# Kernel tuning notes

Measured on AMD Instinct MI355X. Metric: run time of the kernel, lower is better.

The kernel has to match this reference:

```python
import jax, jax.numpy as jnp
import numpy as np
from jax.scipy.special import logsumexp

TEMPERATURE = 0.1
NEG_INF = -1e30


def _l2_normalize(x, eps=1e-12):
    # matches torch F.normalize(dim=1)
    n = jnp.sqrt(jnp.sum(x * x, axis=1, keepdims=True))
    return x / jnp.maximum(n, eps)


def _half_loss(out0, out1, diag):
    # sim matrices [N, N]
    sim_00 = jnp.einsum('nc,mc->nm', out0, out0) / TEMPERATURE
    sim_01 = jnp.einsum('nc,mc->nm', out0, out1) / TEMPERATURE
    positive_loss = -jnp.diagonal(sim_01)            # [N]
    # off-diagonal logsumexp per row (mask diag with -inf)
    neg_00 = logsumexp(jnp.where(diag, NEG_INF, sim_00), axis=1)
    neg_01 = logsumexp(jnp.where(diag, NEG_INF, sim_01), axis=1)
    return positive_loss.mean() + (neg_01 + neg_00).mean()


def setup_inputs() -> dict:
    key = jax.random.key(0)
    k0, k1 = jax.random.split(key)
    N, C = 8192, 128
    return {
        'img_rep': jax.random.normal(k0, (N, C), dtype=jnp.float32),
        'mol_rep': jax.random.normal(k1, (N, C), dtype=jnp.float32),
    }


def reference(img_rep, mol_rep):
    img = _l2_normalize(img_rep)
    mol = _l2_normalize(mol_rep)
    n = img.shape[0]
    diag = jnp.eye(n, dtype=bool)
    loss0 = _half_loss(img, mol, diag)  # mol_from_img
    loss1 = _half_loss(mol, img, diag)  # img_from_mol
    return 0.5 * (loss0 + loss1)
```

## Files before the change

kernel.cpp:

```cpp
#include <hip/hip_runtime.h>
#include <hip/hip_bf16.h>

typedef __attribute__((ext_vector_type(8))) short short8;
typedef __attribute__((ext_vector_type(4))) float floatx4;

#define N_ROWS 8192
#define C_DIM  128
#define CH     8
#define CHUNK  (N_ROWS / CH)
#define NIT    (CHUNK / 64)
#define KSCALE 14.426950408889634f
#define LN2    0.6931471805599453f

__device__ __forceinline__ unsigned int pack_bf16x2(float x, float y) {
    union { float f; unsigned int u; } a, b;
    a.f = x; b.f = y;
    unsigned int ra = a.u + 0x7FFFu + ((a.u >> 16) & 1u);
    unsigned int rb = b.u + 0x7FFFu + ((b.u >> 16) & 1u);
    return (ra >> 16) | ((rb >> 16) << 16);
}
__device__ __forceinline__ float bf2f(unsigned short s) {
    union { unsigned int u; float f; } x; x.u = ((unsigned int)s) << 16;
    return x.f;
}

__global__ __launch_bounds__(256) void norm_kernel(
    const float* __restrict__ img, const float* __restrict__ mol,
    unsigned short* __restrict__ W)
{
    int wave = threadIdx.x >> 6, lane = threadIdx.x & 63;
    int row = blockIdx.x * 4 + wave;
    const float* src = (row < N_ROWS) ? (img + (size_t)row * C_DIM)
                                      : (mol + (size_t)(row - N_ROWS) * C_DIM);
    float2 v = *reinterpret_cast<const float2*>(src + lane * 2);
    float ss = v.x * v.x + v.y * v.y;
    #pragma unroll
    for (int m = 1; m < 64; m <<= 1) ss += __shfl_xor(ss, m);
    float inv = rsqrtf(ss);
    ((unsigned int*)(W + (size_t)row * C_DIM))[lane] =
        pack_bf16x2(v.x * inv, v.y * inv);
}

__global__ __launch_bounds__(256) void pass_kernel(
    const unsigned short* __restrict__ W, float* __restrict__ SE)
{
    __shared__ unsigned short buf[2][64][128];
    int pass = blockIdx.z;
    const unsigned short* X = (pass < 2) ? W : W + (size_t)N_ROWS * C_DIM;
    const unsigned short* Y = (pass == 1 || pass == 2)
                                ? W + (size_t)N_ROWS * C_DIM : W;
    int lane = threadIdx.x & 63, wave = threadIdx.x >> 6;
    int l15 = lane & 15, lg = lane >> 4;
    int rbase = blockIdx.x * 128 + wave * 32;
    int cstart = blockIdx.y * CHUNK;

    short8 af[2][4];
    #pragma unroll
    for (int m = 0; m < 2; ++m)
        #pragma unroll
        for (int k = 0; k < 4; ++k)
            af[m][k] = *reinterpret_cast<const short8*>(
                X + (size_t)(rbase + m * 16 + l15) * C_DIM + k * 32 + lg * 8);

    auto stage = [&](int bsel, int jb) {
        #pragma unroll
        for (int i = 0; i < 4; ++i) {
            int c = i * 4 + wave;
            int r = c * 4 + lg;
            int s = l15 ^ (r & 7);
            const void* gsrc = (const char*)Y + (size_t)(jb + r) * 256 + s * 16;
            void* ldst = (char*)&buf[bsel][0][0] + c * 1024;
            __builtin_amdgcn_global_load_lds(
                (const __attribute__((address_space(1))) unsigned int*)gsrc,
                (__attribute__((address_space(3))) unsigned int*)ldst,
                16, 0, 0);
        }
    };

    float se[2][4] = {{0.f,0.f,0.f,0.f},{0.f,0.f,0.f,0.f}};

    stage(0, cstart);
    int cur = 0;
    for (int it = 0; it < NIT; ++it) {
        if (it + 1 < NIT) {
            stage(cur ^ 1, cstart + (it + 1) * 64);
            asm volatile("s_waitcnt vmcnt(4)" ::: "memory");
        } else {
            asm volatile("s_waitcnt vmcnt(0)" ::: "memory");
        }
        __builtin_amdgcn_s_barrier();
        asm volatile("" ::: "memory");

        #pragma unroll
        for (int n = 0; n < 4; ++n) {
            short8 bk[4];
            #pragma unroll
            for (int k = 0; k < 4; ++k) {
                int row = n * 16 + l15;
                int s = (k * 4 + lg) ^ (l15 & 7);
                bk[k] = *reinterpret_cast<const short8*>(
                    (const char*)&buf[cur][0][0] + row * 256 + s * 16);
            }
            #pragma unroll
            for (int m = 0; m < 2; ++m) {
                floatx4 acc = {0.f, 0.f, 0.f, 0.f};
                #pragma unroll
                for (int k = 0; k < 4; ++k)
                    acc = __builtin_amdgcn_mfma_f32_16x16x32_bf16(
                              af[m][k], bk[k], acc, 0, 0, 0);
                #pragma unroll
                for (int r = 0; r < 4; ++r)
                    se[m][r] += __builtin_amdgcn_exp2f(acc[r] * KSCALE - KSCALE);
            }
        }
        asm volatile("s_waitcnt lgkmcnt(0)" ::: "memory");
        __builtin_amdgcn_sched_barrier(0);
        __builtin_amdgcn_s_barrier();
        cur ^= 1;
    }

    float* SEp = SE + (size_t)pass * N_ROWS;
    #pragma unroll
    for (int m = 0; m < 2; ++m)
        #pragma unroll
        for (int r = 0; r < 4; ++r) {
            float s = se[m][r];
            s += __shfl_xor(s, 1);
            s += __shfl_xor(s, 2);
            s += __shfl_xor(s, 4);
            s += __shfl_xor(s, 8);
            if (l15 == 0)
                atomicAdd(&SEp[rbase + m * 16 + lg * 4 + r], s);
        }
}

__global__ __launch_bounds__(256) void finalize_kernel(
    const unsigned short* __restrict__ W, const float* __restrict__ SE,
    float* __restrict__ out)
{
    __shared__ float partial[4];
    int lane = threadIdx.x & 63, wave = threadIdx.x >> 6;
    int row = blockIdx.x * 4 + wave;
    const unsigned short* a = W + (size_t)row * C_DIM;
    const unsigned short* b = W + (size_t)(N_ROWS + row) * C_DIM;
    float a0 = bf2f(a[lane * 2]), a1 = bf2f(a[lane * 2 + 1]);
    float b0 = bf2f(b[lane * 2]), b1 = bf2f(b[lane * 2 + 1]);
    float d00 = a0 * a0 + a1 * a1;
    float d01 = a0 * b0 + a1 * b1;
    float d11 = b0 * b0 + b1 * b1;
    #pragma unroll
    for (int m = 1; m < 64; m <<= 1) {
        d00 += __shfl_xor(d00, m);
        d01 += __shfl_xor(d01, m);
        d11 += __shfl_xor(d11, m);
    }
    if (lane == 0) {
        float s0 = SE[0 * N_ROWS + row] - __builtin_amdgcn_exp2f(KSCALE * (d00 - 1.f));
        float s1 = SE[1 * N_ROWS + row] - __builtin_amdgcn_exp2f(KSCALE * (d01 - 1.f));
        float s2 = SE[2 * N_ROWS + row] - __builtin_amdgcn_exp2f(KSCALE * (d11 - 1.f));
        float s3 = SE[3 * N_ROWS + row] - __builtin_amdgcn_exp2f(KSCALE * (d01 - 1.f));
        float l0 = LN2 * __builtin_amdgcn_logf(s0) + 10.f;
        float l1 = LN2 * __builtin_amdgcn_logf(s1) + 10.f;
        float l2 = LN2 * __builtin_amdgcn_logf(s2) + 10.f;
        float l3 = LN2 * __builtin_amdgcn_logf(s3) + 10.f;
        partial[wave] = -10.f * d01 + 0.5f * (l0 + l1 + l2 + l3);
    }
    __syncthreads();
    if (threadIdx.x == 0)
        atomicAdd(out, (partial[0] + partial[1] + partial[2] + partial[3])
                         * (1.0f / N_ROWS));
}

extern "C" void kernel_launch(void* const* d_in, const int* in_sizes, int n_in,
                              void* d_out, int out_size, void* d_ws, size_t ws_size,
                              hipStream_t stream)
{
    const float* img = (const float*)d_in[0];
    const float* mol = (const float*)d_in[1];
    float* out = (float*)d_out;
    unsigned short* W = (unsigned short*)d_ws;
    float* SE = (float*)((char*)d_ws + (size_t)2 * N_ROWS * C_DIM * 2);

    hipMemsetAsync(d_out, 0, sizeof(float), stream);
    hipMemsetAsync(SE, 0, (size_t)4 * N_ROWS * sizeof(float), stream);
    norm_kernel<<<dim3(N_ROWS * 2 / 4), 256, 0, stream>>>(img, mol, W);
    pass_kernel<<<dim3(N_ROWS / 128, CH, 4), 256, 0, stream>>>(W, SE);
    finalize_kernel<<<dim3(N_ROWS / 4), 256, 0, stream>>>(W, SE, out);
}
```

Baseline: 171.3 us.

## Exploit similarity symmetry to compute row and column exp-sums in one pass

Each computed tile of exp(similarity) is now used for both its row sums and its column sums. The cross-similarity pass therefore produces both SE[1] and SE[3], and the self-similarity passes compute only upper-triangular tile blocks plus diagonal blocks. This cuts the MFMA and exp work by nearly half. The memsets are folded into the normalization kernel to remove two launches. The price is extra shared-memory atomics for the column partials, more global atomics, and a triangular index mapping in a serial while loop.

```diff
diff --git a/kernel.cpp b/kernel.cpp
--- a/kernel.cpp
+++ b/kernel.cpp
@@ -6,8 +6,7 @@
 
 #define N_ROWS 8192
 #define C_DIM  128
-#define CH     8
-#define CHUNK  (N_ROWS / CH)
+#define CHUNK  512
 #define NIT    (CHUNK / 64)
 #define KSCALE 14.426950408889634f
 #define LN2    0.6931471805599453f
@@ -26,8 +25,14 @@
 
 __global__ __launch_bounds__(256) void norm_kernel(
     const float* __restrict__ img, const float* __restrict__ mol,
-    unsigned short* __restrict__ W)
-{
+    unsigned short* __restrict__ W, float* __restrict__ SE,
+    float* __restrict__ out)
+{
+    if (blockIdx.x < 32) {
+        int t = blockIdx.x * 1024 + threadIdx.x;
+        SE[t] = 0.f; SE[t + 256] = 0.f; SE[t + 512] = 0.f; SE[t + 768] = 0.f;
+        if (blockIdx.x == 0 && threadIdx.x == 0) *out = 0.f;
+    }
     int wave = threadIdx.x >> 6, lane = threadIdx.x & 63;
     int row = blockIdx.x * 4 + wave;
     const float* src = (row < N_ROWS) ? (img + (size_t)row * C_DIM)
@@ -45,14 +50,37 @@
     const unsigned short* __restrict__ W, float* __restrict__ SE)
 {
     __shared__ unsigned short buf[2][64][128];
-    int pass = blockIdx.z;
-    const unsigned short* X = (pass < 2) ? W : W + (size_t)N_ROWS * C_DIM;
-    const unsigned short* Y = (pass == 1 || pass == 2)
-                                ? W + (size_t)N_ROWS * C_DIM : W;
+    __shared__ float colbuf[CHUNK];
+
+    int idx = blockIdx.x;
+    const unsigned short *X, *Y;
+    float *rowSE, *colSE;
+    bool dual;
+    int rb, ch;
+    if (idx < 1024) {
+        rb = idx >> 4; ch = idx & 15;
+        X = W; Y = W + (size_t)N_ROWS * C_DIM;
+        rowSE = SE + 1 * N_ROWS; colSE = SE + 3 * N_ROWS; dual = true;
+    } else {
+        int j = idx - 1024;
+        const unsigned short* M = (j < 544) ? W : W + (size_t)N_ROWS * C_DIM;
+        float* S = (j < 544) ? SE : SE + 2 * N_ROWS;
+        if (j >= 544) j -= 544;
+        X = M; Y = M; rowSE = S; colSE = S;
+        if (j < 64) { rb = j; ch = rb >> 2; dual = false; }
+        else {
+            int j2 = j - 64, p = j2 >> 2;
+            int si = 0, cum = 15;
+            while (p >= cum) { p -= cum; ++si; cum = 15 - si; }
+            int sj = si + 1 + p;
+            rb = si * 4 + (j2 & 3); ch = sj; dual = true;
+        }
+    }
+
     int lane = threadIdx.x & 63, wave = threadIdx.x >> 6;
     int l15 = lane & 15, lg = lane >> 4;
-    int rbase = blockIdx.x * 128 + wave * 32;
-    int cstart = blockIdx.y * CHUNK;
+    int rbase = rb * 128 + wave * 32;
+    int cstart = ch * CHUNK;
 
     short8 af[2][4];
     #pragma unroll
@@ -68,7 +96,7 @@
             int c = i * 4 + wave;
             int r = c * 4 + lg;
             int s = l15 ^ (r & 7);
-            const void* gsrc = (const char*)Y + (size_t)(jb + r) * 256 + s * 16;
+            const void* gsrc = (const char*)Y + (size_t)(cstart + jb + r) * 256 + s * 16;
             void* ldst = (char*)&buf[bsel][0][0] + c * 1024;
             __builtin_amdgcn_global_load_lds(
                 (const __attribute__((address_space(1))) unsigned int*)gsrc,
@@ -77,13 +105,15 @@
         }
     };
 
+    for (int c = threadIdx.x; c < CHUNK; c += 256) colbuf[c] = 0.f;
+
     float se[2][4] = {{0.f,0.f,0.f,0.f},{0.f,0.f,0.f,0.f}};
 
-    stage(0, cstart);
+    stage(0, 0);
     int cur = 0;
     for (int it = 0; it < NIT; ++it) {
         if (it + 1 < NIT) {
-            stage(cur ^ 1, cstart + (it + 1) * 64);
+            stage(cur ^ 1, (it + 1) * 64);
             asm volatile("s_waitcnt vmcnt(4)" ::: "memory");
         } else {
             asm volatile("s_waitcnt vmcnt(0)" ::: "memory");
@@ -91,6 +121,7 @@
         __builtin_amdgcn_s_barrier();
         asm volatile("" ::: "memory");
 
+        float ce[4] = {0.f, 0.f, 0.f, 0.f};
         #pragma unroll
         for (int n = 0; n < 4; ++n) {
             short8 bk[4];
@@ -109,8 +140,21 @@
                     acc = __builtin_amdgcn_mfma_f32_16x16x32_bf16(
                               af[m][k], bk[k], acc, 0, 0, 0);
                 #pragma unroll
-                for (int r = 0; r < 4; ++r)
-                    se[m][r] += __builtin_amdgcn_exp2f(acc[r] * KSCALE - KSCALE);
+                for (int r = 0; r < 4; ++r) {
+                    float e = __builtin_amdgcn_exp2f(acc[r] * KSCALE - KSCALE);
+                    se[m][r] += e;
+                    ce[n] += e;
+                }
+            }
+        }
+        if (dual) {
+            #pragma unroll
+            for (int n = 0; n < 4; ++n) {
+                float c2 = ce[n];
+                c2 += __shfl_xor(c2, 16);
+                c2 += __shfl_xor(c2, 32);
+                if (lg == 0)
+                    atomicAdd(&colbuf[it * 64 + n * 16 + l15], c2);
             }
         }
         asm volatile("s_waitcnt lgkmcnt(0)" ::: "memory");
@@ -119,7 +163,6 @@
         cur ^= 1;
     }
 
-    float* SEp = SE + (size_t)pass * N_ROWS;
     #pragma unroll
     for (int m = 0; m < 2; ++m)
         #pragma unroll
@@ -130,8 +173,12 @@
             s += __shfl_xor(s, 4);
             s += __shfl_xor(s, 8);
             if (l15 == 0)
-                atomicAdd(&SEp[rbase + m * 16 + lg * 4 + r], s);
-        }
+                atomicAdd(&rowSE[rbase + m * 16 + lg * 4 + r], s);
+        }
+    __syncthreads();
+    if (dual)
+        for (int c = threadIdx.x; c < CHUNK; c += 256)
+            atomicAdd(&colSE[cstart + c], colbuf[c]);
 }
 
 __global__ __launch_bounds__(256) void finalize_kernel(
@@ -181,9 +228,7 @@
     unsigned short* W = (unsigned short*)d_ws;
     float* SE = (float*)((char*)d_ws + (size_t)2 * N_ROWS * C_DIM * 2);
 
-    hipMemsetAsync(d_out, 0, sizeof(float), stream);
-    hipMemsetAsync(SE, 0, (size_t)4 * N_ROWS * sizeof(float), stream);
-    norm_kernel<<<dim3(N_ROWS * 2 / 4), 256, 0, stream>>>(img, mol, W);
-    pass_kernel<<<dim3(N_ROWS / 128, CH, 4), 256, 0, stream>>>(W, SE);
+    norm_kernel<<<dim3(N_ROWS * 2 / 4), 256, 0, stream>>>(img, mol, W, SE, out);
+    pass_kernel<<<dim3(1024 + 544 + 544), 256, 0, stream>>>(W, SE);
     finalize_kernel<<<dim3(N_ROWS / 4), 256, 0, stream>>>(W, SE, out);
 }
```

After: 153.4 us. -10.5%, faster.
